# Kernel optimization log

Hardware: AMD Instinct MI355X
Metric: run time of the kernel (lower is better)

The kernel has to match this reference:

```python
import jax, jax.numpy as jnp
import numpy as np

L = 3          # number of Blocks
D = 1024       # embed_dims
H = 16         # headcount
HD = D // H    # head_size = 64
T = 1024       # context_size
V = 32000      # vocabulary_size
B = 2          # batch
EPS = 1e-5


def layernorm(x, g, b):
    m = jnp.mean(x, axis=-1, keepdims=True)
    v = jnp.var(x, axis=-1, keepdims=True)
    return (x - m) * jax.lax.rsqrt(v + EPS) * g + b


def setup_inputs() -> dict:
    key = jax.random.key(0)
    ks = jax.random.split(key, 16)
    s = 0.02
    return {
        "idx": jax.random.randint(ks[0], (B, T), 0, V, dtype=jnp.int64),
        "tok_emb": jax.random.normal(ks[1], (V, D), jnp.float32) * s,
        "pos_emb": jax.random.normal(ks[2], (T, D), jnp.float32) * s,
        # per-layer stacked attention params (equivalent to per-head Linears concatenated)
        "wq": jax.random.normal(ks[3], (L, H, D, HD), jnp.float32) * s,
        "wk": jax.random.normal(ks[4], (L, H, D, HD), jnp.float32) * s,
        "wv": jax.random.normal(ks[5], (L, H, D, HD), jnp.float32) * s,
        "w_proj": jax.random.normal(ks[6], (L, D, D), jnp.float32) * s,
        "b_proj": jnp.zeros((L, D), jnp.float32),
        "w1": jax.random.normal(ks[7], (L, D, 4 * D), jnp.float32) * s,
        "b1": jnp.zeros((L, 4 * D), jnp.float32),
        "w2": jax.random.normal(ks[8], (L, 4 * D, D), jnp.float32) * s,
        "b2": jnp.zeros((L, D), jnp.float32),
        "ln1_g": jnp.ones((L, D), jnp.float32),
        "ln1_b": jnp.zeros((L, D), jnp.float32),
        "ln2_g": jnp.ones((L, D), jnp.float32),
        "ln2_b": jnp.zeros((L, D), jnp.float32),
        "lnf_g": jnp.ones((D,), jnp.float32),
        "lnf_b": jnp.zeros((D,), jnp.float32),
        "w_lm": jax.random.normal(ks[9], (D, V), jnp.float32) * s,
        "b_lm": jnp.zeros((V,), jnp.float32),
    }


def reference(idx, tok_emb, pos_emb, wq, wk, wv, w_proj, b_proj,
              w1, b1, w2, b2, ln1_g, ln1_b, ln2_g, ln2_b,
              lnf_g, lnf_b, w_lm, b_lm):
    Bc, Tc = idx.shape
    x = tok_emb[idx] + pos_emb[:Tc]                  # [B,T,D]
    causal = jnp.tril(jnp.ones((Tc, Tc), dtype=bool))
    scale = HD ** -0.5
    for l in range(L):
        h = layernorm(x, ln1_g[l], ln1_b[l])
        q = jnp.einsum('btd,hdk->bhtk', h, wq[l])
        k = jnp.einsum('btd,hdk->bhtk', h, wk[l])
        v = jnp.einsum('btd,hdk->bhtk', h, wv[l])
        scores = jnp.einsum('bhtk,bhsk->bhts', q, k) * scale
        scores = jnp.where(causal, scores, -jnp.inf)
        w = jax.nn.softmax(scores, axis=-1)          # dropout = identity (eval)
        attn = jnp.einsum('bhts,bhsk->bhtk', w, v)
        attn = attn.transpose(0, 2, 1, 3).reshape(Bc, Tc, H * HD)
        sa = attn @ w_proj[l] + b_proj[l]
        h2 = layernorm(x, ln2_g[l], ln2_b[l])
        ff = jax.nn.relu(h2 @ w1[l] + b1[l]) @ w2[l] + b2[l]
        # faithful to source: NO residual x; y = sa + ffwd only
        x = sa + ff
    x = layernorm(x, lnf_g, lnf_b)
    logits = x @ w_lm + b_lm                         # [B,T,V]
    return logits
```

## Files before the change

### kernel.cpp

```cpp
#include <hip/hip_runtime.h>

#define D_    1024
#define T_    1024
#define H_    16
#define HD_   64
#define NL    3
#define VOC   32000
#define BAT   2
#define MR    (BAT*T_)

typedef unsigned short u16;
typedef unsigned int   u32;
typedef __bf16 bf16x8 __attribute__((ext_vector_type(8)));
typedef float  f32x4  __attribute__((ext_vector_type(4)));

__device__ __forceinline__ u16 f2b(float f){
  u32 u = __float_as_uint(f);
  u += 0x7fffu + ((u >> 16) & 1u);
  return (u16)(u >> 16);
}
__device__ __forceinline__ float blo(u32 w){ return __uint_as_float(w << 16); }
__device__ __forceinline__ float bhi(u32 w){ return __uint_as_float(w & 0xffff0000u); }
__device__ __forceinline__ u32 pk2(float a, float b){ return (u32)f2b(a) | ((u32)f2b(b) << 16); }

__global__ __launch_bounds__(256) void embed_k(const int* __restrict__ idx,
    const float* __restrict__ tok, const float* __restrict__ pos, float* __restrict__ x){
  int bt = blockIdx.x, tid = threadIdx.x;
  int t = bt & (T_-1);
  int tk = idx[bt];
  float4 a = ((const float4*)(tok + (size_t)tk * D_))[tid];
  float4 p = ((const float4*)(pos + (size_t)t  * D_))[tid];
  a.x += p.x; a.y += p.y; a.z += p.z; a.w += p.w;
  ((float4*)(x + (size_t)bt * D_))[tid] = a;
}

__global__ __launch_bounds__(256) void ln_k(const float* __restrict__ x,
    const float* __restrict__ g, const float* __restrict__ b, u16* __restrict__ out){
  int row = blockIdx.x, tid = threadIdx.x;
  float4 v = ((const float4*)(x + (size_t)row * D_))[tid];
  float s = v.x+v.y+v.z+v.w;
  float q = v.x*v.x+v.y*v.y+v.z*v.z+v.w*v.w;
  #pragma unroll
  for (int off = 32; off >= 1; off >>= 1){
    s += __shfl_xor(s, off);
    q += __shfl_xor(q, off);
  }
  __shared__ float ss[4], sq[4];
  int wave = tid >> 6;
  if ((tid & 63) == 0){ ss[wave] = s; sq[wave] = q; }
  __syncthreads();
  s = ss[0]+ss[1]+ss[2]+ss[3];
  q = sq[0]+sq[1]+sq[2]+sq[3];
  float mean = s * (1.f/D_);
  float var  = q * (1.f/D_) - mean*mean;
  float rs = rsqrtf(var + 1e-5f);
  float4 gg = ((const float4*)g)[tid];
  float4 bb = ((const float4*)b)[tid];
  u32 p0 = pk2((v.x-mean)*rs*gg.x+bb.x, (v.y-mean)*rs*gg.y+bb.y);
  u32 p1 = pk2((v.z-mean)*rs*gg.z+bb.z, (v.w-mean)*rs*gg.w+bb.w);
  ((uint2*)(out + (size_t)row * D_))[tid] = make_uint2(p0, p1);
}

__global__ __launch_bounds__(1024) void repack_t_k(const float* __restrict__ src,
    u16* __restrict__ dst, int K, int N, size_t sstride, size_t dstride){
  __shared__ float tile[32][33];
  int l = blockIdx.z;
  const float* s = src + (size_t)l * sstride;
  u16* d = dst + (size_t)l * dstride;
  int n0 = blockIdx.x << 5, k0 = blockIdx.y << 5;
  int tx = threadIdx.x, ty = threadIdx.y;
  tile[ty][tx] = s[(size_t)(k0 + ty) * N + n0 + tx];
  __syncthreads();
  d[(size_t)(n0 + ty) * K + k0 + tx] = f2b(tile[tx][ty]);
}

__global__ __launch_bounds__(1024) void repack_qkv_k(const float* __restrict__ wq,
    const float* __restrict__ wk, const float* __restrict__ wv, u16* __restrict__ dst){
  __shared__ float tile[32][33];
  int l = blockIdx.z;
  int d0 = blockIdx.x << 5;
  int n0 = blockIdx.y << 5;
  int which = n0 >> 10, within = n0 & 1023;
  int hh = within >> 6, hd0 = within & 63;
  const float* src = (which == 0 ? wq : (which == 1 ? wk : wv))
                     + ((size_t)l * H_ + hh) * (D_ * HD_);
  int tx = threadIdx.x, ty = threadIdx.y;
  tile[ty][tx] = src[(size_t)(d0 + ty) * HD_ + hd0 + tx];
  __syncthreads();
  dst[((size_t)l * 3072 + n0 + ty) * D_ + d0 + tx] = f2b(tile[tx][ty]);
}

__global__ __launch_bounds__(256) void gemm_k(
    const u16* __restrict__ A, const u16* __restrict__ Bt,
    const float* __restrict__ bias, const float* __restrict__ resid,
    float* __restrict__ Cf, u16* __restrict__ Cb,
    int M, int N, int K, int relu)
{
  __shared__ u16 Als[128*32];
  __shared__ u16 Bls[128*32];
  int tiles_n = N >> 7;
  int tm = blockIdx.x / tiles_n, tn = blockIdx.x % tiles_n;
  int m0 = tm << 7, n0 = tn << 7;
  int tid = threadIdx.x, lane = tid & 63, wave = tid >> 6;
  int wm = (wave >> 1) << 6, wn = (wave & 1) << 6;
  f32x4 acc[4][4];
  f32x4 zero = {0.f, 0.f, 0.f, 0.f};
  #pragma unroll
  for (int i = 0; i < 4; i++)
    #pragma unroll
    for (int j = 0; j < 4; j++) acc[i][j] = zero;
  int r0 = tid >> 2, c0 = (tid & 3) << 3;
  const u16* Ap = A  + (size_t)(m0 + r0) * K + c0;
  const u16* Bp = Bt + (size_t)(n0 + r0) * K + c0;
  int fr = lane & 15, fq = (lane >> 4) << 3;
  for (int k0 = 0; k0 < K; k0 += 32){
    uint4 a0 = *(const uint4*)(Ap + k0);
    uint4 a1 = *(const uint4*)(Ap + (size_t)64 * K + k0);
    uint4 b0 = *(const uint4*)(Bp + k0);
    uint4 b1 = *(const uint4*)(Bp + (size_t)64 * K + k0);
    __syncthreads();
    *(uint4*)(Als + r0*32 + c0)      = a0;
    *(uint4*)(Als + (64+r0)*32 + c0) = a1;
    *(uint4*)(Bls + r0*32 + c0)      = b0;
    *(uint4*)(Bls + (64+r0)*32 + c0) = b1;
    __syncthreads();
    bf16x8 af[4], bfr[4];
    #pragma unroll
    for (int i = 0; i < 4; i++) af[i]  = *(const bf16x8*)(Als + (wm + i*16 + fr)*32 + fq);
    #pragma unroll
    for (int i = 0; i < 4; i++) bfr[i] = *(const bf16x8*)(Bls + (wn + i*16 + fr)*32 + fq);
    #pragma unroll
    for (int mi = 0; mi < 4; mi++)
      #pragma unroll
      for (int ni = 0; ni < 4; ni++)
        acc[mi][ni] = __builtin_amdgcn_mfma_f32_16x16x32_bf16(af[mi], bfr[ni], acc[mi][ni], 0, 0, 0);
  }
  int cn = lane & 15, rq = (lane >> 4) << 2;
  #pragma unroll
  for (int mi = 0; mi < 4; mi++){
    #pragma unroll
    for (int ni = 0; ni < 4; ni++){
      int c = n0 + wn + ni*16 + cn;
      float bv = bias ? bias[c] : 0.f;
      #pragma unroll
      for (int r = 0; r < 4; r++){
        int rr = m0 + wm + mi*16 + rq + r;
        float v = acc[mi][ni][r] + bv;
        if (resid) v += resid[(size_t)rr * N + c];
        if (relu)  v = fmaxf(v, 0.f);
        if (Cf) Cf[(size_t)rr * N + c] = v;
        if (Cb) Cb[(size_t)rr * N + c] = f2b(v);
      }
    }
  }
}

__global__ __launch_bounds__(256) void attn_k(const u16* __restrict__ qkv, u16* __restrict__ out){
  __shared__ u16 kls[64][72];
  __shared__ u16 vtls[64][72];
  __shared__ u16 pls[4][16][72];
  int bid = blockIdx.x;
  int qt = bid & 15, bh = bid >> 4;
  int h = bh & (H_-1), b = bh >> 4;
  int q0 = qt << 6;
  int tid = threadIdx.x, lane = tid & 63, wave = tid >> 6;
  int fr = lane & 15, fq = (lane >> 4) << 3;
  int cn = fr, rq = (lane >> 4) << 2;

  const u16* qp = qkv + ((size_t)(b*T_ + q0 + wave*16 + fr) * 3072 + h*64);
  bf16x8 qa0 = *(const bf16x8*)(qp + fq);
  bf16x8 qa1 = *(const bf16x8*)(qp + 32 + fq);

  f32x4 acc[4];
  f32x4 zero = {0.f,0.f,0.f,0.f};
  #pragma unroll
  for (int i = 0; i < 4; i++) acc[i] = zero;
  float mrun[4], lrun[4];
  #pragma unroll
  for (int r = 0; r < 4; r++){ mrun[r] = -1e30f; lrun[r] = 0.f; }

  int ldrow = tid >> 3, ldseg = tid & 7;
  const u16* kbase = qkv + ((size_t)(b*T_ + ldrow) * 3072 + 1024 + h*64 + ldseg*8);
  const size_t rstep = (size_t)32 * 3072;

  for (int ch = 0; ch <= qt; ch++){
    const u16* kp = kbase + (size_t)(ch << 6) * 3072;
    uint4 kv0 = *(const uint4*)kp;
    uint4 kv1 = *(const uint4*)(kp + rstep);
    uint4 vv0 = *(const uint4*)(kp + 1024);
    uint4 vv1 = *(const uint4*)(kp + rstep + 1024);
    __syncthreads();
    *(uint4*)(&kls[ldrow][ldseg*8])      = kv0;
    *(uint4*)(&kls[ldrow + 32][ldseg*8]) = kv1;
    union { uint4 u; u16 s[8]; } vu0, vu1; vu0.u = vv0; vu1.u = vv1;
    #pragma unroll
    for (int j = 0; j < 8; j++){
      vtls[ldseg*8 + j][ldrow]      = vu0.s[j];
      vtls[ldseg*8 + j][ldrow + 32] = vu1.s[j];
    }
    __syncthreads();

    f32x4 sf[4];
    #pragma unroll
    for (int ni = 0; ni < 4; ni++) sf[ni] = zero;
    #pragma unroll
    for (int ni = 0; ni < 4; ni++){
      bf16x8 kb0 = *(const bf16x8*)(&kls[ni*16 + fr][fq]);
      bf16x8 kb1 = *(const bf16x8*)(&kls[ni*16 + fr][32 + fq]);
      sf[ni] = __builtin_amdgcn_mfma_f32_16x16x32_bf16(qa0, kb0, sf[ni], 0, 0, 0);
      sf[ni] = __builtin_amdgcn_mfma_f32_16x16x32_bf16(qa1, kb1, sf[ni], 0, 0, 0);
    }

    int s0 = ch << 6;
    float sv[4][4];
    if (ch == qt){
      #pragma unroll
      for (int ni = 0; ni < 4; ni++)
        #pragma unroll
        for (int r = 0; r < 4; r++){
          int srow = s0 + ni*16 + cn;
          int qrow = q0 + wave*16 + rq + r;
          sv[ni][r] = (srow <= qrow) ? sf[ni][r]*0.125f : -1e30f;
        }
    } else {
      #pragma unroll
      for (int ni = 0; ni < 4; ni++)
        #pragma unroll
        for (int r = 0; r < 4; r++) sv[ni][r] = sf[ni][r]*0.125f;
    }

    #pragma unroll
    for (int r = 0; r < 4; r++){
      float mx = fmaxf(fmaxf(sv[0][r], sv[1][r]), fmaxf(sv[2][r], sv[3][r]));
      #pragma unroll
      for (int off = 8; off >= 1; off >>= 1) mx = fmaxf(mx, __shfl_xor(mx, off));
      float mn = fmaxf(mrun[r], mx);
      float al = __expf(mrun[r] - mn);
      mrun[r] = mn;
      float ps = 0.f;
      #pragma unroll
      for (int ni = 0; ni < 4; ni++){
        float p = __expf(sv[ni][r] - mn);
        sv[ni][r] = p; ps += p;
      }
      #pragma unroll
      for (int off = 8; off >= 1; off >>= 1) ps += __shfl_xor(ps, off);
      lrun[r] = lrun[r]*al + ps;
      #pragma unroll
      for (int ni = 0; ni < 4; ni++) acc[ni][r] *= al;
    }

    #pragma unroll
    for (int ni = 0; ni < 4; ni++)
      #pragma unroll
      for (int r = 0; r < 4; r++)
        pls[wave][rq + r][ni*16 + cn] = f2b(sv[ni][r]);
    __syncthreads();

    #pragma unroll
    for (int kk = 0; kk < 2; kk++){
      bf16x8 pa = *(const bf16x8*)(&pls[wave][fr][kk*32 + fq]);
      #pragma unroll
      for (int di = 0; di < 4; di++){
        bf16x8 vb = *(const bf16x8*)(&vtls[di*16 + fr][kk*32 + fq]);
        acc[di] = __builtin_amdgcn_mfma_f32_16x16x32_bf16(pa, vb, acc[di], 0, 0, 0);
      }
    }
  }

  u16* ob = out + ((size_t)(b*T_ + q0 + wave*16) * D_ + h*64);
  #pragma unroll
  for (int r = 0; r < 4; r++){
    float inv = 1.f / lrun[r];
    #pragma unroll
    for (int di = 0; di < 4; di++)
      ob[(size_t)(rq + r) * D_ + di*16 + cn] = f2b(acc[di][r] * inv);
  }
}

extern "C" void kernel_launch(void* const* d_in, const int* in_sizes, int n_in,
                              void* d_out, int out_size, void* d_ws, size_t ws_size,
                              hipStream_t stream){
  (void)in_sizes; (void)n_in; (void)out_size; (void)ws_size;
  const int*   idx     = (const int*)  d_in[0];
  const float* tok_emb = (const float*)d_in[1];
  const float* pos_emb = (const float*)d_in[2];
  const float* wq      = (const float*)d_in[3];
  const float* wk      = (const float*)d_in[4];
  const float* wv      = (const float*)d_in[5];
  const float* w_proj  = (const float*)d_in[6];
  const float* b_proj  = (const float*)d_in[7];
  const float* w1      = (const float*)d_in[8];
  const float* b1      = (const float*)d_in[9];
  const float* w2      = (const float*)d_in[10];
  const float* b2      = (const float*)d_in[11];
  const float* ln1g    = (const float*)d_in[12];
  const float* ln1b    = (const float*)d_in[13];
  const float* ln2g    = (const float*)d_in[14];
  const float* ln2b    = (const float*)d_in[15];
  const float* lnfg    = (const float*)d_in[16];
  const float* lnfb    = (const float*)d_in[17];
  const float* w_lm    = (const float*)d_in[18];
  const float* b_lm    = (const float*)d_in[19];

  char* ws = (char*)d_ws;
  size_t off = 0;
  auto alloc = [&](size_t bytes)->char*{
    char* p = ws + off; off += (bytes + 255) & ~(size_t)255; return p;
  };
  u16*   qkvT  = (u16*)  alloc((size_t)NL*3072*1024*2);
  u16*   projT = (u16*)  alloc((size_t)NL*1024*1024*2);
  u16*   w1T   = (u16*)  alloc((size_t)NL*4096*1024*2);
  u16*   w2T   = (u16*)  alloc((size_t)NL*1024*4096*2);
  u16*   wlmT  = (u16*)  alloc((size_t)VOC*1024*2);
  float* x     = (float*)alloc((size_t)MR*1024*4);
  u16*   hbuf  = (u16*)  alloc((size_t)MR*1024*2);
  u16*   qkvb  = (u16*)  alloc((size_t)MR*3072*2);
  u16*   attnb = (u16*)  alloc((size_t)MR*1024*2);
  float* sa    = (float*)alloc((size_t)MR*1024*4);
  u16*   ff1   = (u16*)  alloc((size_t)MR*4096*2);

  auto gemm = [&](const u16* A, const u16* Bt, const float* bias, const float* resid,
                  float* Cf, u16* Cb, int M, int N, int K, int relu){
    int blocks = (M >> 7) * (N >> 7);
    gemm_k<<<dim3(blocks), dim3(256), 0, stream>>>(A, Bt, bias, resid, Cf, Cb, M, N, K, relu);
  };

  repack_qkv_k<<<dim3(32,96,3),  dim3(32,32), 0, stream>>>(wq, wk, wv, qkvT);
  repack_t_k  <<<dim3(32,32,3),  dim3(32,32), 0, stream>>>(w_proj, projT, 1024, 1024, (size_t)1048576, (size_t)1048576);
  repack_t_k  <<<dim3(128,32,3), dim3(32,32), 0, stream>>>(w1, w1T, 1024, 4096, (size_t)4194304, (size_t)4194304);
  repack_t_k  <<<dim3(32,128,3), dim3(32,32), 0, stream>>>(w2, w2T, 4096, 1024, (size_t)4194304, (size_t)4194304);
  repack_t_k  <<<dim3(1000,32,1),dim3(32,32), 0, stream>>>(w_lm, wlmT, 1024, VOC, (size_t)0, (size_t)0);

  embed_k<<<dim3(MR), dim3(256), 0, stream>>>(idx, tok_emb, pos_emb, x);

  for (int l = 0; l < NL; l++){
    ln_k<<<dim3(MR), dim3(256), 0, stream>>>(x, ln1g + l*1024, ln1b + l*1024, hbuf);
    gemm(hbuf, qkvT + (size_t)l*3072*1024, nullptr, nullptr, nullptr, qkvb, MR, 3072, 1024, 0);
    attn_k<<<dim3(512), dim3(256), 0, stream>>>(qkvb, attnb);
    gemm(attnb, projT + (size_t)l*1048576, b_proj + l*1024, nullptr, sa, nullptr, MR, 1024, 1024, 0);
    ln_k<<<dim3(MR), dim3(256), 0, stream>>>(x, ln2g + l*1024, ln2b + l*1024, hbuf);
    gemm(hbuf, w1T + (size_t)l*4194304, b1 + l*4096, nullptr, nullptr, ff1, MR, 4096, 1024, 1);
    gemm(ff1, w2T + (size_t)l*4194304, b2 + l*1024, sa, x, nullptr, MR, 1024, 4096, 0);
  }
  ln_k<<<dim3(MR), dim3(256), 0, stream>>>(x, lnfg, lnfb, hbuf);
  gemm(hbuf, wlmT, b_lm, nullptr, (float*)d_out, nullptr, MR, VOC, 1024, 0);
}
```

Before: 1.625 ms.

## Use direct global-to-LDS loads with swizzled layout and grouped tile order in GEMM

The GEMM now copies A and B tiles from global memory straight into LDS with global_load_lds 16-byte transfers, so the data no longer passes through registers. The LDS layout is XOR-swizzled per row pair to cut bank conflicts on the MFMA fragment reads. Blocks are remapped into groups of 8 column tiles to improve L2 reuse of B. Without a wait on the vmcnt counter before the barrier, correctness depends on the compiler inserting that wait. There is still no double buffering.

```diff
diff --git a/kernel.cpp b/kernel.cpp
--- a/kernel.cpp
+++ b/kernel.cpp
@@ -22,6 +22,12 @@
 __device__ __forceinline__ float blo(u32 w){ return __uint_as_float(w << 16); }
 __device__ __forceinline__ float bhi(u32 w){ return __uint_as_float(w & 0xffff0000u); }
 __device__ __forceinline__ u32 pk2(float a, float b){ return (u32)f2b(a) | ((u32)f2b(b) << 16); }
+
+__device__ __forceinline__ void gload16(const u16* g, u16* l){
+  __builtin_amdgcn_global_load_lds(
+      (const __attribute__((address_space(1))) void*)g,
+      (__attribute__((address_space(3))) void*)l, 16, 0, 0);
+}
 
 __global__ __launch_bounds__(256) void embed_k(const int* __restrict__ idx,
     const float* __restrict__ tok, const float* __restrict__ pos, float* __restrict__ x){
@@ -96,10 +102,25 @@
     float* __restrict__ Cf, u16* __restrict__ Cb,
     int M, int N, int K, int relu)
 {
-  __shared__ u16 Als[128*32];
-  __shared__ u16 Bls[128*32];
-  int tiles_n = N >> 7;
-  int tm = blockIdx.x / tiles_n, tn = blockIdx.x % tiles_n;
+  __shared__ __attribute__((aligned(16))) u16 Als[128*32];
+  __shared__ __attribute__((aligned(16))) u16 Bls[128*32];
+  int tiles_m = M >> 7, tiles_n = N >> 7;
+  int tm, tn;
+  {
+    const int GN = 8;
+    int full = tiles_n / GN;
+    int fullsz = full * GN * tiles_m;
+    int bid = blockIdx.x;
+    if (bid < fullsz){
+      int g = bid / (GN * tiles_m);
+      int r = bid % (GN * tiles_m);
+      tm = r / GN; tn = g * GN + (r % GN);
+    } else {
+      int r = bid - fullsz;
+      int remn = tiles_n - full * GN;
+      tm = r / remn; tn = full * GN + (r % remn);
+    }
+  }
   int m0 = tm << 7, n0 = tn << 7;
   int tid = threadIdx.x, lane = tid & 63, wave = tid >> 6;
   int wm = (wave >> 1) << 6, wn = (wave & 1) << 6;
@@ -109,26 +130,34 @@
   for (int i = 0; i < 4; i++)
     #pragma unroll
     for (int j = 0; j < 4; j++) acc[i][j] = zero;
-  int r0 = tid >> 2, c0 = (tid & 3) << 3;
-  const u16* Ap = A  + (size_t)(m0 + r0) * K + c0;
-  const u16* Bp = Bt + (size_t)(n0 + r0) * K + c0;
-  int fr = lane & 15, fq = (lane >> 4) << 3;
+
+  int lrow = lane >> 2, lseg = lane & 3;
+  int arow = wave*16 + lrow;
+  int ssw  = (arow >> 1) & 3;
+  int scol = ((lseg ^ ssw) << 3);
+  const u16* Ag0 = A  + (size_t)(m0 + arow) * K + scol;
+  const u16* Ag1 = Ag0 + (size_t)64 * K;
+  const u16* Bg0 = Bt + (size_t)(n0 + arow) * K + scol;
+  const u16* Bg1 = Bg0 + (size_t)64 * K;
+  u16* Al0 = Als + wave*512;
+  u16* Al1 = Als + 64*32 + wave*512;
+  u16* Bl0 = Bls + wave*512;
+  u16* Bl1 = Bls + 64*32 + wave*512;
+
+  int fr = lane & 15;
+  int fqs = (((lane >> 4) ^ ((fr >> 1) & 3)) << 3);
   for (int k0 = 0; k0 < K; k0 += 32){
-    uint4 a0 = *(const uint4*)(Ap + k0);
-    uint4 a1 = *(const uint4*)(Ap + (size_t)64 * K + k0);
-    uint4 b0 = *(const uint4*)(Bp + k0);
-    uint4 b1 = *(const uint4*)(Bp + (size_t)64 * K + k0);
-    __syncthreads();
-    *(uint4*)(Als + r0*32 + c0)      = a0;
-    *(uint4*)(Als + (64+r0)*32 + c0) = a1;
-    *(uint4*)(Bls + r0*32 + c0)      = b0;
-    *(uint4*)(Bls + (64+r0)*32 + c0) = b1;
+    __syncthreads();
+    gload16(Ag0 + k0, Al0);
+    gload16(Ag1 + k0, Al1);
+    gload16(Bg0 + k0, Bl0);
+    gload16(Bg1 + k0, Bl1);
     __syncthreads();
     bf16x8 af[4], bfr[4];
     #pragma unroll
-    for (int i = 0; i < 4; i++) af[i]  = *(const bf16x8*)(Als + (wm + i*16 + fr)*32 + fq);
-    #pragma unroll
-    for (int i = 0; i < 4; i++) bfr[i] = *(const bf16x8*)(Bls + (wn + i*16 + fr)*32 + fq);
+    for (int i = 0; i < 4; i++) af[i]  = *(const bf16x8*)(Als + (wm + i*16 + fr)*32 + fqs);
+    #pragma unroll
+    for (int i = 0; i < 4; i++) bfr[i] = *(const bf16x8*)(Bls + (wn + i*16 + fr)*32 + fqs);
     #pragma unroll
     for (int mi = 0; mi < 4; mi++)
       #pragma unroll
```

New measurement: 1.682 ms. 3.5% more time.
